# Kernel tuning notes

Hardware: AMD Instinct MI355X
Metric: run time of the kernel (lower is better)

## Reference

```python
import jax, jax.numpy as jnp
import numpy as np

B, V, S, H, I, L, NH = 32, 50, 64, 256, 512, 2, 4
VOCAB, SEGV, AGEV = 30000, 2, 144
EPS = 1e-12


def _ln(x, g, b):
    m = jnp.mean(x, axis=-1, keepdims=True)
    v = jnp.mean((x - m) ** 2, axis=-1, keepdims=True)
    return (x - m) / jnp.sqrt(v + EPS) * g + b


def _sinusoid_table(max_pos, hidden):
    pos = np.arange(max_pos, dtype=np.float32)[:, None]
    idx = np.arange(hidden, dtype=np.float32)[None, :]
    ang = pos / np.power(10000.0, 2.0 * idx / hidden)
    tab = np.where((np.arange(hidden) % 2 == 0)[None, :], np.sin(ang), np.cos(ang))
    return jnp.asarray(tab, dtype=jnp.float32)


def setup_inputs() -> dict:
    key = jax.random.key(0)
    ks = iter(jax.random.split(key, 48))

    def nrm(shape, s=0.02):
        return jax.random.normal(next(ks), shape, dtype=jnp.float32) * s

    inp = {
        "word": jax.random.randint(next(ks), (B, V, S), 0, VOCAB),
        "age": jax.random.randint(next(ks), (B, V, S), 0, AGEV),
        "seg": jax.random.randint(next(ks), (B, V, S), 0, SEGV),
        "posi": jax.random.randint(next(ks), (B, V, S), 0, S),
        "mask": jnp.ones((B, V, S), dtype=jnp.float32),
        "token": 0,
        "word_emb": nrm((VOCAB, H)),
        "seg_emb": nrm((SEGV, H)),
        "age_emb": nrm((AGEV, H)),
        "posi_emb": _sinusoid_table(S, H),
        "emb_ln_g": jnp.ones((H,), jnp.float32),
        "emb_ln_b": jnp.zeros((H,), jnp.float32),
        "qw": nrm((L, H, H)), "qb": jnp.zeros((L, H), jnp.float32),
        "kw": nrm((L, H, H)), "kb": jnp.zeros((L, H), jnp.float32),
        "vw": nrm((L, H, H)), "vb": jnp.zeros((L, H), jnp.float32),
        "ow": nrm((L, H, H)), "ob": jnp.zeros((L, H), jnp.float32),
        "attn_ln_g": jnp.ones((L, H), jnp.float32),
        "attn_ln_b": jnp.zeros((L, H), jnp.float32),
        "iw": nrm((L, H, I)), "ib": jnp.zeros((L, I), jnp.float32),
        "outw": nrm((L, I, H)), "outb": jnp.zeros((L, H), jnp.float32),
        "out_ln_g": jnp.ones((L, H), jnp.float32),
        "out_ln_b": jnp.zeros((L, H), jnp.float32),
        "pool_w": nrm((H, H)), "pool_b": jnp.zeros((H,), jnp.float32),
    }
    return inp


def reference(word, age, seg, posi, mask, token,
              word_emb, seg_emb, age_emb, posi_emb, emb_ln_g, emb_ln_b,
              qw, qb, kw, kb, vw, vb, ow, ob, attn_ln_g, attn_ln_b,
              iw, ib, outw, outb, out_ln_g, out_ln_b, pool_w, pool_b):
    # token embeddings: word + seg + age + sinusoidal position, then LayerNorm
    emb = word_emb[word] + seg_emb[seg] + age_emb[age] + posi_emb[posi]  # [B,V,S,H]
    x = _ln(emb, emb_ln_g, emb_ln_b)
    N = B * V
    x = x.reshape(N, S, H)  # vectorize the per-visit loop over the batch axis
    am = ((1.0 - mask) * -10000.0).reshape(N, 1, 1, S)  # additive attention mask
    d = H // NH
    scale = 1.0 / jnp.sqrt(jnp.float32(d))
    n_layers = qw.shape[0]
    for l in range(n_layers):
        q = (x @ qw[l] + qb[l]).reshape(N, S, NH, d)
        k = (x @ kw[l] + kb[l]).reshape(N, S, NH, d)
        v = (x @ vw[l] + vb[l]).reshape(N, S, NH, d)
        scores = jnp.einsum("bqhd,bkhd->bhqk", q, k) * scale + am
        probs = jax.nn.softmax(scores, axis=-1)  # dropout = identity (eval)
        ctx = jnp.einsum("bhqk,bkhd->bqhd", probs, v).reshape(N, S, H)
        a = _ln(ctx @ ow[l] + ob[l] + x, attn_ln_g[l], attn_ln_b[l])
        h = jax.nn.gelu(a @ iw[l] + ib[l], approximate=False)
        x = _ln(h @ outw[l] + outb[l] + a, out_ln_g[l], out_ln_b[l])
    first = x[:, 0].reshape(B, V, H)  # pooler with token=False: hidden[:, 0]
    return jnp.tanh(first @ pool_w + pool_b)  # [B, V, H]
```

## Files before the change

### kernel.cpp

```cpp
#include <hip/hip_runtime.h>
#include <math.h>

typedef __attribute__((ext_vector_type(8))) short short8;
typedef __attribute__((ext_vector_type(4))) short short4v;
typedef __attribute__((ext_vector_type(4))) float f32x4;

#define M_TOT 102400

__device__ __forceinline__ unsigned short f2b(float f) {
  unsigned u = __float_as_uint(f);
  return (unsigned short)((u + 0x7fffu + ((u >> 16) & 1u)) >> 16);
}
__device__ __forceinline__ float b2f(unsigned short h) {
  return __uint_as_float(((unsigned)h) << 16);
}
__device__ __forceinline__ f32x4 mfma16(short8 a, short8 b, f32x4 c) {
  return __builtin_amdgcn_mfma_f32_16x16x32_bf16(a, b, c, 0, 0, 0);
}
template <int STRIDE>
__device__ __forceinline__ short8 lds8(const short* buf, int row, int k) {
  int idx = (row * STRIDE + k) ^ ((row & 7) << 3);
  return *(const short8*)(buf + idx);
}
template <int STRIDE>
__device__ __forceinline__ void ldsw(short* buf, int row, int col, unsigned short v) {
  buf[(row * STRIDE + col) ^ ((row & 7) << 3)] = (short)v;
}
__device__ __forceinline__ float red16sum(float v) {
  v += __shfl_xor(v, 1); v += __shfl_xor(v, 2);
  v += __shfl_xor(v, 4); v += __shfl_xor(v, 8);
  return v;
}
__device__ __forceinline__ float red16max(float v) {
  v = fmaxf(v, __shfl_xor(v, 1)); v = fmaxf(v, __shfl_xor(v, 2));
  v = fmaxf(v, __shfl_xor(v, 4)); v = fmaxf(v, __shfl_xor(v, 8));
  return v;
}

__device__ __forceinline__ void stage16k(const short* __restrict__ g, short* l,
                                         int w, int lane) {
  const char* gb = (const char*)g + w * 4096 + lane * 16;
  char* lb = (char*)l + w * 4096;
#pragma unroll
  for (int c = 0; c < 4; ++c)
    __builtin_amdgcn_global_load_lds(
        (const __attribute__((address_space(1))) unsigned int*)(gb + c * 1024),
        (__attribute__((address_space(3))) unsigned int*)(lb + c * 1024), 16, 0, 0);
}

template <int KB>
__device__ __forceinline__ void gemm_core(const short* __restrict__ A, int lda,
                                          const short* __restrict__ Wimg,
                                          short* sB, f32x4 acc[16], int r0,
                                          int w, int lane, int l15, int g4) {
  short8 af[KB];
#pragma unroll
  for (int kk = 0; kk < KB; ++kk)
    af[kk] = *(const short8*)(A + (size_t)(r0 + l15) * lda + kk * 32 + g4 * 8);
  stage16k(Wimg, sB, w, lane);
  stage16k(Wimg + 8192, sB + 8192, w, lane);
#pragma unroll
  for (int kb = 0; kb < KB; ++kb) {
    if (kb + 1 < KB) {
      asm volatile("s_waitcnt vmcnt(4)" ::: "memory");
    } else {
      asm volatile("s_waitcnt vmcnt(0)" ::: "memory");
    }
    __builtin_amdgcn_s_barrier();
    __builtin_amdgcn_sched_barrier(0);
    const short* cur = sB + (kb & 1) * 8192;
#pragma unroll
    for (int tc = 0; tc < 16; ++tc) {
      int row = tc * 16 + l15;
      short8 bf = *(const short8*)(cur + ((row * 32 + g4 * 8) ^ ((row & 7) << 3)));
      acc[tc] = mfma16(af[kb], bf, acc[tc]);
    }
    if (kb + 2 < KB) {
      __builtin_amdgcn_sched_barrier(0);
      __builtin_amdgcn_s_barrier();
      stage16k(Wimg + (kb + 2) * 8192, sB + (kb & 1) * 8192, w, lane);
    }
  }
}

__device__ __forceinline__ void ln_epi(f32x4 acc[16], short* x,
                                       const float* __restrict__ bias,
                                       const float* __restrict__ g_,
                                       const float* __restrict__ b_,
                                       int r0, int l15, int g4) {
  float s1[4] = {0.f, 0.f, 0.f, 0.f}, s2[4] = {0.f, 0.f, 0.f, 0.f};
#pragma unroll
  for (int tc = 0; tc < 16; ++tc) {
    int col = tc * 16 + l15;
    float bv = bias[col];
#pragma unroll
    for (int r = 0; r < 4; ++r) {
      float v = acc[tc][r] + bv + b2f((unsigned short)x[(r0 + g4 * 4 + r) * 256 + col]);
      acc[tc][r] = v;
      s1[r] += v; s2[r] += v * v;
    }
  }
  float mean[4], rstd[4];
#pragma unroll
  for (int r = 0; r < 4; ++r) {
    float a = red16sum(s1[r]), q = red16sum(s2[r]);
    mean[r] = a * (1.f / 256.f);
    rstd[r] = rsqrtf(q * (1.f / 256.f) - mean[r] * mean[r] + 1e-12f);
  }
#pragma unroll
  for (int tc = 0; tc < 16; ++tc) {
    int col = tc * 16 + l15;
    float gv = g_[col], bv = b_[col];
#pragma unroll
    for (int r = 0; r < 4; ++r)
      x[(r0 + g4 * 4 + r) * 256 + col] =
          (short)f2b((acc[tc][r] - mean[r]) * rstd[r] * gv + bv);
  }
}

__global__ void prep_w(const float* __restrict__ qw, const float* __restrict__ kw,
                       const float* __restrict__ vw, const float* __restrict__ ow,
                       const float* __restrict__ iw, const float* __restrict__ outw,
                       const float* __restrict__ pw, short* __restrict__ ws) {
  int t = blockIdx.x * 256 + threadIdx.x;
  float val; int base, n, k;
  if (t < 524288) {
    int which = t >> 17, r = t & 131071;
    int ly = r >> 16, e = r & 65535;
    n = e >> 8; k = e & 255;
    const float* m = which == 0 ? qw : which == 1 ? kw : which == 2 ? vw : ow;
    val = m[(ly * 256 + k) * 256 + n];
    base = which * 131072 + ly * 65536;
  } else if (t < 786432) {
    int e = t - 524288;
    int ly = e >> 17, f = e & 131071, g2 = f >> 16, e2 = f & 65535;
    n = e2 >> 8; k = e2 & 255;
    val = iw[(ly * 256 + k) * 512 + g2 * 256 + n];
    base = 524288 + ly * 131072 + g2 * 65536;
  } else if (t < 1048576) {
    int e = t - 786432;
    int ly = e >> 17, f = e & 131071;
    n = f >> 9; k = f & 511;
    val = outw[(ly * 512 + k) * 256 + n];
    base = 786432 + ly * 131072;
  } else {
    int e = t - 1048576;
    n = e >> 8; k = e & 255;
    val = pw[k * 256 + n];
    base = 1048576;
  }
  int pos = ((n * 32 + (k & 31)) ^ ((n & 7) << 3));
  ws[base + (k >> 5) * 8192 + pos] = (short)f2b(val);
}

__global__ __launch_bounds__(256) void emb_k(
    const int* __restrict__ word, const int* __restrict__ age,
    const int* __restrict__ seg, const int* __restrict__ posi,
    const float* __restrict__ we, const float* __restrict__ se,
    const float* __restrict__ ae, const float* __restrict__ pe,
    const float* __restrict__ g, const float* __restrict__ b,
    short* __restrict__ x) {
  int w = threadIdx.x >> 6, lane = threadIdx.x & 63;
  int t = blockIdx.x * 4 + w;
  int wi = word[t], gi = seg[t], ai = age[t], pi = posi[t];
  f32x4 e = ((const f32x4*)(we + wi * 256))[lane];
  f32x4 tv = ((const f32x4*)(se + gi * 256))[lane]; e = e + tv;
  tv = ((const f32x4*)(ae + ai * 256))[lane]; e = e + tv;
  tv = ((const f32x4*)(pe + pi * 256))[lane]; e = e + tv;
  float s1 = e[0] + e[1] + e[2] + e[3];
  float s2 = e[0] * e[0] + e[1] * e[1] + e[2] * e[2] + e[3] * e[3];
#pragma unroll
  for (int m = 1; m < 64; m <<= 1) { s1 += __shfl_xor(s1, m); s2 += __shfl_xor(s2, m); }
  float mean = s1 * (1.f / 256.f);
  float rstd = rsqrtf(s2 * (1.f / 256.f) - mean * mean + 1e-12f);
  f32x4 gv = ((const f32x4*)g)[lane];
  f32x4 bv = ((const f32x4*)b)[lane];
  short4v pk;
#pragma unroll
  for (int j = 0; j < 4; ++j) pk[j] = (short)f2b((e[j] - mean) * rstd * gv[j] + bv[j]);
  *(short4v*)(x + t * 256 + lane * 4) = pk;
}

__global__ __launch_bounds__(256) void qkv3_k(
    const short* __restrict__ x, const short* __restrict__ img,
    const float* __restrict__ qb_, const float* __restrict__ kb_,
    const float* __restrict__ vb_,
    short* __restrict__ q, short* __restrict__ k2, short* __restrict__ vt, int ly) {
  __shared__ __align__(16) short sB[16384];
  int w = threadIdx.x >> 6, lane = threadIdx.x & 63;
  int l15 = lane & 15, g4 = lane >> 4;
  int y = blockIdx.y;
  int r0 = blockIdx.x * 64 + w * 16;
  const short* W = img + y * 131072 + ly * 65536;
  const float* bias = (y == 0 ? qb_ : y == 1 ? kb_ : vb_) + ly * 256;
  f32x4 acc[16];
#pragma unroll
  for (int i = 0; i < 16; ++i) acc[i] = f32x4{0.f, 0.f, 0.f, 0.f};
  gemm_core<8>(x, 256, W, sB, acc, r0, w, lane, l15, g4);
  if (y < 2) {
    short* out = y ? k2 : q;
#pragma unroll
    for (int tc = 0; tc < 16; ++tc) {
      int col = tc * 16 + l15;
      float bv = bias[col];
#pragma unroll
      for (int r = 0; r < 4; ++r)
        out[(r0 + g4 * 4 + r) * 256 + col] = (short)f2b(acc[tc][r] + bv);
    }
  } else {
#pragma unroll
    for (int tc = 0; tc < 16; ++tc) {
      int col = tc * 16 + l15;
      float bv = bias[col];
#pragma unroll
      for (int r = 0; r < 4; ++r) {
        int tok = r0 + g4 * 4 + r;
        vt[(tok >> 6) * 16384 + col * 64 + (tok & 63)] = (short)f2b(acc[tc][r] + bv);
      }
    }
  }
}

__global__ __launch_bounds__(256) void attn_k(
    const short* __restrict__ q, const short* __restrict__ k,
    const short* __restrict__ vt, short* __restrict__ ctx,
    const float* __restrict__ mask) {
  __shared__ __align__(16) short sP[16384];
  int w = threadIdx.x >> 6, lane = threadIdx.x & 63;
  int l15 = lane & 15, g4 = lane >> 4;
  int n = blockIdx.x;
  const f32x4 zero4 = {0.f, 0.f, 0.f, 0.f};
  short* sPw = sP + w * 4096;

  float amvr[4];
#pragma unroll
  for (int tc = 0; tc < 4; ++tc)
    amvr[tc] = (1.f - mask[n * 64 + tc * 16 + l15]) * -10000.f;

  const short* qn = q + (size_t)n * 16384;
  const short* kn = k + (size_t)n * 16384;
  const short* vtn = vt + (size_t)n * 16384;

  short8 qa[4][2];
#pragma unroll
  for (int st = 0; st < 4; ++st)
#pragma unroll
    for (int ks = 0; ks < 2; ++ks)
      qa[st][ks] = *(const short8*)(qn + (st * 16 + l15) * 256 + w * 64 + ks * 32 + g4 * 8);
  f32x4 sacc[4][4];
#pragma unroll
  for (int st = 0; st < 4; ++st)
#pragma unroll
    for (int tc = 0; tc < 4; ++tc) sacc[st][tc] = zero4;
#pragma unroll
  for (int ks = 0; ks < 2; ++ks)
#pragma unroll
    for (int tc = 0; tc < 4; ++tc) {
      short8 kf = *(const short8*)(kn + (tc * 16 + l15) * 256 + w * 64 + ks * 32 + g4 * 8);
#pragma unroll
      for (int st = 0; st < 4; ++st) sacc[st][tc] = mfma16(qa[st][ks], kf, sacc[st][tc]);
    }
#pragma unroll
  for (int st = 0; st < 4; ++st)
#pragma unroll
    for (int r = 0; r < 4; ++r) {
      float pv[4];
      float mx = -1e30f;
#pragma unroll
      for (int tc = 0; tc < 4; ++tc) {
        float sv = sacc[st][tc][r] * 0.125f + amvr[tc];
        pv[tc] = sv;
        mx = fmaxf(mx, sv);
      }
      mx = red16max(mx);
      float sm = 0.f;
#pragma unroll
      for (int tc = 0; tc < 4; ++tc) {
        float e = __expf(pv[tc] - mx);
        pv[tc] = e;
        sm += e;
      }
      sm = red16sum(sm);
      float inv = 1.f / sm;
#pragma unroll
      for (int tc = 0; tc < 4; ++tc)
        ldsw<64>(sPw, st * 16 + g4 * 4 + r, tc * 16 + l15, f2b(pv[tc] * inv));
    }
  __syncthreads();

  f32x4 cacc[4][4];
#pragma unroll
  for (int st = 0; st < 4; ++st)
#pragma unroll
    for (int tc = 0; tc < 4; ++tc) cacc[st][tc] = zero4;
#pragma unroll
  for (int ks = 0; ks < 2; ++ks) {
    short8 pa[4];
#pragma unroll
    for (int st = 0; st < 4; ++st) pa[st] = lds8<64>(sPw, st * 16 + l15, ks * 32 + g4 * 8);
#pragma unroll
    for (int tc = 0; tc < 4; ++tc) {
      short8 vf = *(const short8*)(vtn + (w * 64 + tc * 16 + l15) * 64 + ks * 32 + g4 * 8);
#pragma unroll
      for (int st = 0; st < 4; ++st) cacc[st][tc] = mfma16(pa[st], vf, cacc[st][tc]);
    }
  }
#pragma unroll
  for (int st = 0; st < 4; ++st)
#pragma unroll
    for (int tc = 0; tc < 4; ++tc)
#pragma unroll
      for (int r = 0; r < 4; ++r)
        ctx[((size_t)n * 64 + st * 16 + g4 * 4 + r) * 256 + w * 64 + tc * 16 + l15] =
            (short)f2b(cacc[st][tc][r]);
}

__global__ __launch_bounds__(256) void oln_k(
    const short* __restrict__ ctx, const short* __restrict__ img,
    const float* __restrict__ bias, short* __restrict__ x,
    const float* __restrict__ g_, const float* __restrict__ b_) {
  __shared__ __align__(16) short sB[16384];
  int w = threadIdx.x >> 6, lane = threadIdx.x & 63;
  int l15 = lane & 15, g4 = lane >> 4;
  int r0 = blockIdx.x * 64 + w * 16;
  f32x4 acc[16];
#pragma unroll
  for (int i = 0; i < 16; ++i) acc[i] = f32x4{0.f, 0.f, 0.f, 0.f};
  gemm_core<8>(ctx, 256, img, sB, acc, r0, w, lane, l15, g4);
  ln_epi(acc, x, bias, g_, b_, r0, l15, g4);
}

__global__ __launch_bounds__(256) void ffn1_k(
    const short* __restrict__ x, const short* __restrict__ img,
    const float* __restrict__ bias, short* __restrict__ h) {
  __shared__ __align__(16) short sB[16384];
  int w = threadIdx.x >> 6, lane = threadIdx.x & 63;
  int l15 = lane & 15, g4 = lane >> 4;
  int y = blockIdx.y;
  int r0 = blockIdx.x * 64 + w * 16;
  f32x4 acc[16];
#pragma unroll
  for (int i = 0; i < 16; ++i) acc[i] = f32x4{0.f, 0.f, 0.f, 0.f};
  gemm_core<8>(x, 256, img + y * 65536, sB, acc, r0, w, lane, l15, g4);
  const float* bs = bias + y * 256;
#pragma unroll
  for (int tc = 0; tc < 16; ++tc) {
    int col = tc * 16 + l15;
    float bv = bs[col];
#pragma unroll
    for (int r = 0; r < 4; ++r) {
      float v = acc[tc][r] + bv;
      v = 0.5f * v * (1.f + erff(v * 0.70710678118f));
      h[(r0 + g4 * 4 + r) * 512 + y * 256 + col] = (short)f2b(v);
    }
  }
}

__global__ __launch_bounds__(256) void ffn2_k(
    const short* __restrict__ h, const short* __restrict__ img,
    const float* __restrict__ bias, short* __restrict__ x,
    const float* __restrict__ g_, const float* __restrict__ b_) {
  __shared__ __align__(16) short sB[16384];
  int w = threadIdx.x >> 6, lane = threadIdx.x & 63;
  int l15 = lane & 15, g4 = lane >> 4;
  int r0 = blockIdx.x * 64 + w * 16;
  f32x4 acc[16];
#pragma unroll
  for (int i = 0; i < 16; ++i) acc[i] = f32x4{0.f, 0.f, 0.f, 0.f};
  gemm_core<16>(h, 512, img, sB, acc, r0, w, lane, l15, g4);
  ln_epi(acc, x, bias, g_, b_, r0, l15, g4);
}

__global__ __launch_bounds__(256) void pool_k(
    const short* __restrict__ x, const short* __restrict__ img,
    const float* __restrict__ pb, float* __restrict__ out) {
  __shared__ __align__(16) short sB[16384];
  int w = threadIdx.x >> 6, lane = threadIdx.x & 63;
  int l15 = lane & 15, g4 = lane >> 4;
  int r0 = blockIdx.x * 64 + w * 16;
  f32x4 acc[16];
#pragma unroll
  for (int i = 0; i < 16; ++i) acc[i] = f32x4{0.f, 0.f, 0.f, 0.f};
  gemm_core<8>(x, 16384, img, sB, acc, r0, w, lane, l15, g4);
#pragma unroll
  for (int tc = 0; tc < 16; ++tc) {
    int col = tc * 16 + l15;
    float bv = pb[col];
#pragma unroll
    for (int r = 0; r < 4; ++r)
      out[(size_t)(r0 + g4 * 4 + r) * 256 + col] = tanhf(acc[tc][r] + bv);
  }
}

extern "C" void kernel_launch(void* const* d_in, const int* in_sizes, int n_in,
                              void* d_out, int out_size, void* d_ws, size_t ws_size,
                              hipStream_t stream) {
  const int* word = (const int*)d_in[0];
  const int* age = (const int*)d_in[1];
  const int* seg = (const int*)d_in[2];
  const int* posi = (const int*)d_in[3];
  const float* mask = (const float*)d_in[4];
  const float* word_emb = (const float*)d_in[6];
  const float* seg_emb = (const float*)d_in[7];
  const float* age_emb = (const float*)d_in[8];
  const float* posi_emb = (const float*)d_in[9];
  const float* emb_g = (const float*)d_in[10];
  const float* emb_b = (const float*)d_in[11];
  const float* qw = (const float*)d_in[12];
  const float* qb = (const float*)d_in[13];
  const float* kw = (const float*)d_in[14];
  const float* kb = (const float*)d_in[15];
  const float* vw = (const float*)d_in[16];
  const float* vb = (const float*)d_in[17];
  const float* ow = (const float*)d_in[18];
  const float* ob = (const float*)d_in[19];
  const float* attn_g = (const float*)d_in[20];
  const float* attn_b = (const float*)d_in[21];
  const float* iw = (const float*)d_in[22];
  const float* ib = (const float*)d_in[23];
  const float* outw = (const float*)d_in[24];
  const float* outb = (const float*)d_in[25];
  const float* out_g = (const float*)d_in[26];
  const float* out_b = (const float*)d_in[27];
  const float* pool_w = (const float*)d_in[28];
  const float* pool_b = (const float*)d_in[29];
  short* ws = (short*)d_ws;

  short* xb_ = ws + 1114112;
  short* qbuf = xb_ + 26214400;
  short* kbuf = qbuf + 26214400;
  short* vtbuf = kbuf + 26214400;
  short* hbuf = qbuf;

  prep_w<<<4352, 256, 0, stream>>>(qw, kw, vw, ow, iw, outw, pool_w, ws);
  emb_k<<<25600, 256, 0, stream>>>(word, age, seg, posi, word_emb, seg_emb,
                                   age_emb, posi_emb, emb_g, emb_b, xb_);
  for (int ly = 0; ly < 2; ++ly) {
    qkv3_k<<<dim3(1600, 3), 256, 0, stream>>>(xb_, ws, qb, kb, vb, qbuf, kbuf,
                                              vtbuf, ly);
    attn_k<<<1600, 256, 0, stream>>>(qbuf, kbuf, vtbuf, qbuf, mask);
    oln_k<<<1600, 256, 0, stream>>>(qbuf, ws + 393216 + ly * 65536, ob + ly * 256,
                                    xb_, attn_g + ly * 256, attn_b + ly * 256);
    ffn1_k<<<dim3(1600, 2), 256, 0, stream>>>(xb_, ws + 524288 + ly * 131072,
                                              ib + ly * 512, hbuf);
    ffn2_k<<<1600, 256, 0, stream>>>(hbuf, ws + 786432 + ly * 131072,
                                     outb + ly * 256, xb_, out_g + ly * 256,
                                     out_b + ly * 256);
  }
  pool_k<<<25, 256, 0, stream>>>(xb_, ws + 1048576, pool_b, (float*)d_out);
}
```

Before: 670.2 us.

## Stream weight fragments from global into registers and retile GEMMs to 16-row blocks

Replaces the LDS-staged weight GEMM core with a register-based one. Each wave loads a pre-swizzled MFMA-fragment weight slice straight from global memory (cached), double-buffered in registers. Blocks now cover 16 rows with the four waves splitting the 256 output columns, so grids grow fourfold and LDS barriers in the K loop are gone. Epilogues stage results through a small swizzled LDS tile for coalesced 16-byte stores, and LayerNorm reduces across waves through shared partial sums. The trade-off is much less reuse of each weight fetch per block and extra cache traffic, in exchange for more parallelism and fewer barriers.

```diff
diff --git a/kernel.cpp b/kernel.cpp
--- a/kernel.cpp
+++ b/kernel.cpp
@@ -4,8 +4,6 @@
 typedef __attribute__((ext_vector_type(8))) short short8;
 typedef __attribute__((ext_vector_type(4))) short short4v;
 typedef __attribute__((ext_vector_type(4))) float f32x4;
-
-#define M_TOT 102400
 
 __device__ __forceinline__ unsigned short f2b(float f) {
   unsigned u = __float_as_uint(f);
@@ -37,84 +35,29 @@
   return v;
 }
 
-__device__ __forceinline__ void stage16k(const short* __restrict__ g, short* l,
-                                         int w, int lane) {
-  const char* gb = (const char*)g + w * 4096 + lane * 16;
-  char* lb = (char*)l + w * 4096;
-#pragma unroll
-  for (int c = 0; c < 4; ++c)
-    __builtin_amdgcn_global_load_lds(
-        (const __attribute__((address_space(1))) unsigned int*)(gb + c * 1024),
-        (__attribute__((address_space(3))) unsigned int*)(lb + c * 1024), 16, 0, 0);
-}
-
 template <int KB>
-__device__ __forceinline__ void gemm_core(const short* __restrict__ A, int lda,
-                                          const short* __restrict__ Wimg,
-                                          short* sB, f32x4 acc[16], int r0,
-                                          int w, int lane, int l15, int g4) {
+__device__ __forceinline__ void gemm_reg(const short* __restrict__ A, int lda,
+                                         int k0, const short* __restrict__ Wslice,
+                                         f32x4 acc[4], int r0, int lane) {
+  int l15 = lane & 15, g4 = lane >> 4;
   short8 af[KB];
 #pragma unroll
   for (int kk = 0; kk < KB; ++kk)
-    af[kk] = *(const short8*)(A + (size_t)(r0 + l15) * lda + kk * 32 + g4 * 8);
-  stage16k(Wimg, sB, w, lane);
-  stage16k(Wimg + 8192, sB + 8192, w, lane);
+    af[kk] = *(const short8*)(A + (size_t)(r0 + l15) * lda + k0 + kk * 32 + g4 * 8);
+  short8 bf[2][4];
+#pragma unroll
+  for (int t = 0; t < 4; ++t)
+    bf[0][t] = *(const short8*)(Wslice + t * 512 + lane * 8);
 #pragma unroll
   for (int kb = 0; kb < KB; ++kb) {
     if (kb + 1 < KB) {
-      asm volatile("s_waitcnt vmcnt(4)" ::: "memory");
-    } else {
-      asm volatile("s_waitcnt vmcnt(0)" ::: "memory");
-    }
-    __builtin_amdgcn_s_barrier();
-    __builtin_amdgcn_sched_barrier(0);
-    const short* cur = sB + (kb & 1) * 8192;
-#pragma unroll
-    for (int tc = 0; tc < 16; ++tc) {
-      int row = tc * 16 + l15;
-      short8 bf = *(const short8*)(cur + ((row * 32 + g4 * 8) ^ ((row & 7) << 3)));
-      acc[tc] = mfma16(af[kb], bf, acc[tc]);
-    }
-    if (kb + 2 < KB) {
-      __builtin_amdgcn_sched_barrier(0);
-      __builtin_amdgcn_s_barrier();
-      stage16k(Wimg + (kb + 2) * 8192, sB + (kb & 1) * 8192, w, lane);
-    }
-  }
-}
-
-__device__ __forceinline__ void ln_epi(f32x4 acc[16], short* x,
-                                       const float* __restrict__ bias,
-                                       const float* __restrict__ g_,
-                                       const float* __restrict__ b_,
-                                       int r0, int l15, int g4) {
-  float s1[4] = {0.f, 0.f, 0.f, 0.f}, s2[4] = {0.f, 0.f, 0.f, 0.f};
-#pragma unroll
-  for (int tc = 0; tc < 16; ++tc) {
-    int col = tc * 16 + l15;
-    float bv = bias[col];
-#pragma unroll
-    for (int r = 0; r < 4; ++r) {
-      float v = acc[tc][r] + bv + b2f((unsigned short)x[(r0 + g4 * 4 + r) * 256 + col]);
-      acc[tc][r] = v;
-      s1[r] += v; s2[r] += v * v;
-    }
-  }
-  float mean[4], rstd[4];
-#pragma unroll
-  for (int r = 0; r < 4; ++r) {
-    float a = red16sum(s1[r]), q = red16sum(s2[r]);
-    mean[r] = a * (1.f / 256.f);
-    rstd[r] = rsqrtf(q * (1.f / 256.f) - mean[r] * mean[r] + 1e-12f);
-  }
-#pragma unroll
-  for (int tc = 0; tc < 16; ++tc) {
-    int col = tc * 16 + l15;
-    float gv = g_[col], bv = b_[col];
-#pragma unroll
-    for (int r = 0; r < 4; ++r)
-      x[(r0 + g4 * 4 + r) * 256 + col] =
-          (short)f2b((acc[tc][r] - mean[r]) * rstd[r] * gv + bv);
+#pragma unroll
+      for (int t = 0; t < 4; ++t)
+        bf[(kb + 1) & 1][t] =
+            *(const short8*)(Wslice + (kb + 1) * 2048 + t * 512 + lane * 8);
+    }
+#pragma unroll
+    for (int t = 0; t < 4; ++t) acc[t] = mfma16(af[kb], bf[kb & 1][t], acc[t]);
   }
 }
 
@@ -123,34 +66,36 @@
                        const float* __restrict__ iw, const float* __restrict__ outw,
                        const float* __restrict__ pw, short* __restrict__ ws) {
   int t = blockIdx.x * 256 + threadIdx.x;
-  float val; int base, n, k;
+  float val; int base, n, k, K;
   if (t < 524288) {
     int which = t >> 17, r = t & 131071;
     int ly = r >> 16, e = r & 65535;
-    n = e >> 8; k = e & 255;
+    n = e >> 8; k = e & 255; K = 256;
     const float* m = which == 0 ? qw : which == 1 ? kw : which == 2 ? vw : ow;
     val = m[(ly * 256 + k) * 256 + n];
     base = which * 131072 + ly * 65536;
   } else if (t < 786432) {
     int e = t - 524288;
-    int ly = e >> 17, f = e & 131071, g2 = f >> 16, e2 = f & 65535;
-    n = e2 >> 8; k = e2 & 255;
-    val = iw[(ly * 256 + k) * 512 + g2 * 256 + n];
-    base = 524288 + ly * 131072 + g2 * 65536;
+    int ly = e >> 17, f = e & 131071;
+    n = f >> 8; k = f & 255; K = 256;
+    val = iw[(ly * 256 + k) * 512 + n];
+    base = 524288 + ly * 131072;
   } else if (t < 1048576) {
     int e = t - 786432;
     int ly = e >> 17, f = e & 131071;
-    n = f >> 9; k = f & 511;
+    n = f >> 9; k = f & 511; K = 512;
     val = outw[(ly * 512 + k) * 256 + n];
     base = 786432 + ly * 131072;
   } else {
     int e = t - 1048576;
-    n = e >> 8; k = e & 255;
+    n = e >> 8; k = e & 255; K = 256;
     val = pw[k * 256 + n];
     base = 1048576;
   }
-  int pos = ((n * 32 + (k & 31)) ^ ((n & 7) << 3));
-  ws[base + (k >> 5) * 8192 + pos] = (short)f2b(val);
+  int s = n >> 6, tt = (n >> 4) & 3;
+  int lane = (n & 15) | (((k >> 3) & 3) << 4);
+  int j = k & 7;
+  ws[base + s * (K * 64) + (k >> 5) * 2048 + tt * 512 + lane * 8 + j] = (short)f2b(val);
 }
 
 __global__ __launch_bounds__(256) void emb_k(
@@ -186,37 +131,57 @@
     const float* __restrict__ qb_, const float* __restrict__ kb_,
     const float* __restrict__ vb_,
     short* __restrict__ q, short* __restrict__ k2, short* __restrict__ vt, int ly) {
-  __shared__ __align__(16) short sB[16384];
-  int w = threadIdx.x >> 6, lane = threadIdx.x & 63;
+  __shared__ __align__(16) short sT[4096];
+  int tid = threadIdx.x, w = tid >> 6, lane = tid & 63;
   int l15 = lane & 15, g4 = lane >> 4;
   int y = blockIdx.y;
-  int r0 = blockIdx.x * 64 + w * 16;
-  const short* W = img + y * 131072 + ly * 65536;
+  int r0 = blockIdx.x * 16;
+  const short* Wslice = img + y * 131072 + ly * 65536 + w * 16384;
   const float* bias = (y == 0 ? qb_ : y == 1 ? kb_ : vb_) + ly * 256;
-  f32x4 acc[16];
-#pragma unroll
-  for (int i = 0; i < 16; ++i) acc[i] = f32x4{0.f, 0.f, 0.f, 0.f};
-  gemm_core<8>(x, 256, W, sB, acc, r0, w, lane, l15, g4);
+  f32x4 acc[4];
+#pragma unroll
+  for (int i = 0; i < 4; ++i) acc[i] = f32x4{0.f, 0.f, 0.f, 0.f};
+  gemm_reg<8>(x, 256, 0, Wslice, acc, r0, lane);
   if (y < 2) {
-    short* out = y ? k2 : q;
-#pragma unroll
-    for (int tc = 0; tc < 16; ++tc) {
-      int col = tc * 16 + l15;
+#pragma unroll
+    for (int t = 0; t < 4; ++t) {
+      int col = w * 64 + t * 16 + l15;
       float bv = bias[col];
 #pragma unroll
-      for (int r = 0; r < 4; ++r)
-        out[(r0 + g4 * 4 + r) * 256 + col] = (short)f2b(acc[tc][r] + bv);
+      for (int r = 0; r < 4; ++r) {
+        int row = g4 * 4 + r;
+        sT[(row * 256 + col) ^ ((row & 7) << 3)] = (short)f2b(acc[t][r] + bv);
+      }
+    }
+    __syncthreads();
+    short* out = (y ? k2 : q) + (size_t)r0 * 256;
+#pragma unroll
+    for (int i = 0; i < 2; ++i) {
+      int j = i * 256 + tid;
+      int row = j >> 5, c8 = j & 31;
+      short8 v = *(const short8*)(sT + ((row * 256 + c8 * 8) ^ ((row & 7) << 3)));
+      *(short8*)(out + j * 8) = v;
     }
   } else {
 #pragma unroll
-    for (int tc = 0; tc < 16; ++tc) {
-      int col = tc * 16 + l15;
-      float bv = bias[col];
+    for (int t = 0; t < 4; ++t) {
+      int d = w * 64 + t * 16 + l15;
+      float bv = bias[d];
 #pragma unroll
       for (int r = 0; r < 4; ++r) {
-        int tok = r0 + g4 * 4 + r;
-        vt[(tok >> 6) * 16384 + col * 64 + (tok & 63)] = (short)f2b(acc[tc][r] + bv);
+        int tl = g4 * 4 + r;
+        sT[d * 16 + (tl ^ ((d & 1) << 3))] = (short)f2b(acc[t][r] + bv);
       }
+    }
+    __syncthreads();
+    int seq = r0 >> 6, tb = r0 & 63;
+    short* dst = vt + (size_t)seq * 16384 + tb;
+#pragma unroll
+    for (int i = 0; i < 2; ++i) {
+      int j = i * 256 + tid;
+      int d = j >> 1, t8 = j & 1;
+      short8 v = *(const short8*)(sT + d * 16 + ((t8 ^ (d & 1)) * 8));
+      *(short8*)(dst + d * 64 + t8 * 8) = v;
     }
   }
 }
@@ -315,44 +280,124 @@
             (short)f2b(cacc[st][tc][r]);
 }
 
+__device__ __forceinline__ void ln_block(f32x4 acc[4], short* __restrict__ x,
+                                         short* sT, float (*part)[16][4],
+                                         const float* __restrict__ bias,
+                                         const float* __restrict__ g_,
+                                         const float* __restrict__ b_,
+                                         int r0, int w, int tid, int l15, int g4) {
+  const short* xsrc = x + (size_t)r0 * 256;
+#pragma unroll
+  for (int i = 0; i < 2; ++i) {
+    int j = i * 256 + tid;
+    int row = j >> 5, c8 = j & 31;
+    short8 v = *(const short8*)(xsrc + j * 8);
+    *(short8*)(sT + ((row * 256 + c8 * 8) ^ ((row & 7) << 3))) = v;
+  }
+  __syncthreads();
+  float s1[4] = {0.f, 0.f, 0.f, 0.f}, s2[4] = {0.f, 0.f, 0.f, 0.f};
+#pragma unroll
+  for (int t = 0; t < 4; ++t) {
+    int col = w * 64 + t * 16 + l15;
+    float bv = bias[col];
+#pragma unroll
+    for (int r = 0; r < 4; ++r) {
+      int row = g4 * 4 + r;
+      float v = acc[t][r] + bv +
+                b2f((unsigned short)sT[(row * 256 + col) ^ ((row & 7) << 3)]);
+      acc[t][r] = v;
+      s1[r] += v; s2[r] += v * v;
+    }
+  }
+#pragma unroll
+  for (int r = 0; r < 4; ++r) {
+    float a = red16sum(s1[r]), qq = red16sum(s2[r]);
+    if (l15 == 0) {
+      part[0][g4 * 4 + r][w] = a;
+      part[1][g4 * 4 + r][w] = qq;
+    }
+  }
+  __syncthreads();
+  float mean[4], rstd[4];
+#pragma unroll
+  for (int r = 0; r < 4; ++r) {
+    int row = g4 * 4 + r;
+    float a = part[0][row][0] + part[0][row][1] + part[0][row][2] + part[0][row][3];
+    float qq = part[1][row][0] + part[1][row][1] + part[1][row][2] + part[1][row][3];
+    mean[r] = a * (1.f / 256.f);
+    rstd[r] = rsqrtf(qq * (1.f / 256.f) - mean[r] * mean[r] + 1e-12f);
+  }
+#pragma unroll
+  for (int t = 0; t < 4; ++t) {
+    int col = w * 64 + t * 16 + l15;
+    float gv = g_[col], bv = b_[col];
+#pragma unroll
+    for (int r = 0; r < 4; ++r) {
+      int row = g4 * 4 + r;
+      sT[(row * 256 + col) ^ ((row & 7) << 3)] =
+          (short)f2b((acc[t][r] - mean[r]) * rstd[r] * gv + bv);
+    }
+  }
+  __syncthreads();
+  short* xdst = x + (size_t)r0 * 256;
+#pragma unroll
+  for (int i = 0; i < 2; ++i) {
+    int j = i * 256 + tid;
+    int row = j >> 5, c8 = j & 31;
+    short8 v = *(const short8*)(sT + ((row * 256 + c8 * 8) ^ ((row & 7) << 3)));
+    *(short8*)(xdst + j * 8) = v;
+  }
+}
+
 __global__ __launch_bounds__(256) void oln_k(
     const short* __restrict__ ctx, const short* __restrict__ img,
     const float* __restrict__ bias, short* __restrict__ x,
     const float* __restrict__ g_, const float* __restrict__ b_) {
-  __shared__ __align__(16) short sB[16384];
-  int w = threadIdx.x >> 6, lane = threadIdx.x & 63;
-  int l15 = lane & 15, g4 = lane >> 4;
-  int r0 = blockIdx.x * 64 + w * 16;
-  f32x4 acc[16];
-#pragma unroll
-  for (int i = 0; i < 16; ++i) acc[i] = f32x4{0.f, 0.f, 0.f, 0.f};
-  gemm_core<8>(ctx, 256, img, sB, acc, r0, w, lane, l15, g4);
-  ln_epi(acc, x, bias, g_, b_, r0, l15, g4);
+  __shared__ __align__(16) short sT[4096];
+  __shared__ float part[2][16][4];
+  int tid = threadIdx.x, w = tid >> 6, lane = tid & 63;
+  int l15 = lane & 15, g4 = lane >> 4;
+  int r0 = blockIdx.x * 16;
+  f32x4 acc[4];
+#pragma unroll
+  for (int i = 0; i < 4; ++i) acc[i] = f32x4{0.f, 0.f, 0.f, 0.f};
+  gemm_reg<8>(ctx, 256, 0, img + w * 16384, acc, r0, lane);
+  ln_block(acc, x, sT, part, bias, g_, b_, r0, w, tid, l15, g4);
 }
 
 __global__ __launch_bounds__(256) void ffn1_k(
     const short* __restrict__ x, const short* __restrict__ img,
     const float* __restrict__ bias, short* __restrict__ h) {
-  __shared__ __align__(16) short sB[16384];
-  int w = threadIdx.x >> 6, lane = threadIdx.x & 63;
+  __shared__ __align__(16) short sT[4096];
+  int tid = threadIdx.x, w = tid >> 6, lane = tid & 63;
   int l15 = lane & 15, g4 = lane >> 4;
   int y = blockIdx.y;
-  int r0 = blockIdx.x * 64 + w * 16;
-  f32x4 acc[16];
-#pragma unroll
-  for (int i = 0; i < 16; ++i) acc[i] = f32x4{0.f, 0.f, 0.f, 0.f};
-  gemm_core<8>(x, 256, img + y * 65536, sB, acc, r0, w, lane, l15, g4);
+  int r0 = blockIdx.x * 16;
+  f32x4 acc[4];
+#pragma unroll
+  for (int i = 0; i < 4; ++i) acc[i] = f32x4{0.f, 0.f, 0.f, 0.f};
+  gemm_reg<8>(x, 256, 0, img + (y * 4 + w) * 16384, acc, r0, lane);
   const float* bs = bias + y * 256;
 #pragma unroll
-  for (int tc = 0; tc < 16; ++tc) {
-    int col = tc * 16 + l15;
+  for (int t = 0; t < 4; ++t) {
+    int col = w * 64 + t * 16 + l15;
     float bv = bs[col];
 #pragma unroll
     for (int r = 0; r < 4; ++r) {
-      float v = acc[tc][r] + bv;
+      float v = acc[t][r] + bv;
       v = 0.5f * v * (1.f + erff(v * 0.70710678118f));
-      h[(r0 + g4 * 4 + r) * 512 + y * 256 + col] = (short)f2b(v);
-    }
+      int row = g4 * 4 + r;
+      sT[(row * 256 + col) ^ ((row & 7) << 3)] = (short)f2b(v);
+    }
+  }
+  __syncthreads();
+  short* dst = h + (size_t)r0 * 512 + y * 256;
+#pragma unroll
+  for (int i = 0; i < 2; ++i) {
+    int j = i * 256 + tid;
+    int row = j >> 5, c8 = j & 31;
+    short8 v = *(const short8*)(sT + ((row * 256 + c8 * 8) ^ ((row & 7) << 3)));
+    *(short8*)(dst + row * 512 + c8 * 8) = v;
   }
 }
 
@@ -360,35 +405,36 @@
     const short* __restrict__ h, const short* __restrict__ img,
     const float* __restrict__ bias, short* __restrict__ x,
     const float* __restrict__ g_, const float* __restrict__ b_) {
-  __shared__ __align__(16) short sB[16384];
-  int w = threadIdx.x >> 6, lane = threadIdx.x & 63;
-  int l15 = lane & 15, g4 = lane >> 4;
-  int r0 = blockIdx.x * 64 + w * 16;
-  f32x4 acc[16];
-#pragma unroll
-  for (int i = 0; i < 16; ++i) acc[i] = f32x4{0.f, 0.f, 0.f, 0.f};
-  gemm_core<16>(h, 512, img, sB, acc, r0, w, lane, l15, g4);
-  ln_epi(acc, x, bias, g_, b_, r0, l15, g4);
+  __shared__ __align__(16) short sT[4096];
+  __shared__ float part[2][16][4];
+  int tid = threadIdx.x, w = tid >> 6, lane = tid & 63;
+  int l15 = lane & 15, g4 = lane >> 4;
+  int r0 = blockIdx.x * 16;
+  f32x4 acc[4];
+#pragma unroll
+  for (int i = 0; i < 4; ++i) acc[i] = f32x4{0.f, 0.f, 0.f, 0.f};
+  gemm_reg<8>(h, 512, 0, img + w * 32768, acc, r0, lane);
+  gemm_reg<8>(h, 512, 256, img + w * 32768 + 16384, acc, r0, lane);
+  ln_block(acc, x, sT, part, bias, g_, b_, r0, w, tid, l15, g4);
 }
 
 __global__ __launch_bounds__(256) void pool_k(
     const short* __restrict__ x, const short* __restrict__ img,
     const float* __restrict__ pb, float* __restrict__ out) {
-  __shared__ __align__(16) short sB[16384];
-  int w = threadIdx.x >> 6, lane = threadIdx.x & 63;
-  int l15 = lane & 15, g4 = lane >> 4;
-  int r0 = blockIdx.x * 64 + w * 16;
-  f32x4 acc[16];
-#pragma unroll
-  for (int i = 0; i < 16; ++i) acc[i] = f32x4{0.f, 0.f, 0.f, 0.f};
-  gemm_core<8>(x, 16384, img, sB, acc, r0, w, lane, l15, g4);
-#pragma unroll
-  for (int tc = 0; tc < 16; ++tc) {
-    int col = tc * 16 + l15;
+  int tid = threadIdx.x, w = tid >> 6, lane = tid & 63;
+  int l15 = lane & 15, g4 = lane >> 4;
+  int r0 = blockIdx.x * 16;
+  f32x4 acc[4];
+#pragma unroll
+  for (int i = 0; i < 4; ++i) acc[i] = f32x4{0.f, 0.f, 0.f, 0.f};
+  gemm_reg<8>(x, 16384, 0, img + w * 16384, acc, r0, lane);
+#pragma unroll
+  for (int t = 0; t < 4; ++t) {
+    int col = w * 64 + t * 16 + l15;
     float bv = pb[col];
 #pragma unroll
     for (int r = 0; r < 4; ++r)
-      out[(size_t)(r0 + g4 * 4 + r) * 256 + col] = tanhf(acc[tc][r] + bv);
+      out[(size_t)(r0 + g4 * 4 + r) * 256 + col] = tanhf(acc[t][r] + bv);
   }
 }
 
@@ -436,16 +482,16 @@
   emb_k<<<25600, 256, 0, stream>>>(word, age, seg, posi, word_emb, seg_emb,
                                    age_emb, posi_emb, emb_g, emb_b, xb_);
   for (int ly = 0; ly < 2; ++ly) {
-    qkv3_k<<<dim3(1600, 3), 256, 0, stream>>>(xb_, ws, qb, kb, vb, qbuf, kbuf,
+    qkv3_k<<<dim3(6400, 3), 256, 0, stream>>>(xb_, ws, qb, kb, vb, qbuf, kbuf,
                                               vtbuf, ly);
     attn_k<<<1600, 256, 0, stream>>>(qbuf, kbuf, vtbuf, qbuf, mask);
-    oln_k<<<1600, 256, 0, stream>>>(qbuf, ws + 393216 + ly * 65536, ob + ly * 256,
+    oln_k<<<6400, 256, 0, stream>>>(qbuf, ws + 393216 + ly * 65536, ob + ly * 256,
                                     xb_, attn_g + ly * 256, attn_b + ly * 256);
-    ffn1_k<<<dim3(1600, 2), 256, 0, stream>>>(xb_, ws + 524288 + ly * 131072,
+    ffn1_k<<<dim3(6400, 2), 256, 0, stream>>>(xb_, ws + 524288 + ly * 131072,
                                               ib + ly * 512, hbuf);
-    ffn2_k<<<1600, 256, 0, stream>>>(hbuf, ws + 786432 + ly * 131072,
+    ffn2_k<<<6400, 256, 0, stream>>>(hbuf, ws + 786432 + ly * 131072,
                                      outb + ly * 256, xb_, out_g + ly * 256,
                                      out_b + ly * 256);
   }
-  pool_k<<<25, 256, 0, stream>>>(xb_, ws + 1048576, pool_b, (float*)d_out);
-}
+  pool_k<<<100, 256, 0, stream>>>(xb_, ws + 1048576, pool_b, (float*)d_out);
+}
```

Result: slower. 943.7 us (+40.8%).
